# Optimization experiments

Hardware: AMD Instinct MI355X
Metric: run time of the kernel (lower is better)

## Reference

```python
import jax, jax.numpy as jnp
import numpy as np

N_NODES = 20000
N_EDGES = 320000
IN_CH = 256
HID_CH = 256   # 2 * out_channels
OUT_CH = 128


def gcn_conv(x, edge_index, W, b, n_nodes):
    """PyG GCNConv: linear transform, add self-loops, sym-normalized scatter-add."""
    x = x @ W  # [N, C_out]
    loop = jnp.arange(n_nodes, dtype=edge_index.dtype)
    row = jnp.concatenate([edge_index[0], loop])  # source nodes
    col = jnp.concatenate([edge_index[1], loop])  # destination nodes
    deg = jax.ops.segment_sum(jnp.ones_like(col, dtype=x.dtype), col,
                              num_segments=n_nodes)
    deg_inv_sqrt = jnp.where(deg > 0, jax.lax.rsqrt(deg), 0.0)
    norm = deg_inv_sqrt[row] * deg_inv_sqrt[col]  # [E+N]
    msg = x[row] * norm[:, None]                  # gather + scale
    out = jax.ops.segment_sum(msg, col, num_segments=n_nodes)  # scatter-add
    return out + b


def setup_inputs() -> dict:
    key = jax.random.key(0)
    k1, k2, k3, k4, k5 = jax.random.split(key, 5)
    doc_embeds = jax.random.normal(k1, (N_NODES, IN_CH), dtype=jnp.float32)
    edge_index = jax.random.randint(k2, (2, N_EDGES), 0, N_NODES, dtype=jnp.int64)
    # Glorot-style init for GCN weights, zero bias (PyG defaults)
    s1 = 1.0 / np.sqrt(IN_CH)
    s2 = 1.0 / np.sqrt(HID_CH)
    W1 = jax.random.uniform(k3, (IN_CH, HID_CH), jnp.float32, -s1, s1)
    b1 = jnp.zeros((HID_CH,), jnp.float32)
    W2 = jax.random.uniform(k4, (HID_CH, OUT_CH), jnp.float32, -s2, s2)
    b2 = jnp.zeros((OUT_CH,), jnp.float32)
    return {"doc_embeds": doc_embeds, "edge_index": edge_index,
            "W1": W1, "b1": b1, "W2": W2, "b2": b2}


def reference(doc_embeds, edge_index, W1, b1, W2, b2):
    n = doc_embeds.shape[0]
    x = jax.nn.relu(gcn_conv(doc_embeds, edge_index, W1, b1, n))
    x = gcn_conv(x, edge_index, W2, b2, n)
    return x
```

## Files before the change

### kernel.cpp

```cpp
#include <hip/hip_runtime.h>
#include <math.h>

#define N_NODES 20000
#define N_EDGES 320000
#define IN_CH   256
#define HID_CH  256
#define OUT_CH  128
#define CAP     64
#define GK      256

typedef __attribute__((ext_vector_type(8))) short short8;
typedef __attribute__((ext_vector_type(8))) unsigned short ushort8;
typedef __attribute__((ext_vector_type(4))) unsigned short ushort4v;
typedef __attribute__((ext_vector_type(2))) unsigned short ushort2v;
typedef __attribute__((ext_vector_type(4))) float floatx4;
typedef __attribute__((ext_vector_type(2))) float floatx2;
typedef __attribute__((ext_vector_type(2))) _Float16 half2v;

static __device__ __forceinline__ unsigned short f2bf(float f) {
    unsigned int u = __float_as_uint(f);
    u += 0x7FFFu + ((u >> 16) & 1u);
    return (unsigned short)(u >> 16);
}
static __device__ __forceinline__ float bf2f(unsigned short h) {
    return __uint_as_float(((unsigned int)h) << 16);
}

__global__ __launch_bounds__(256)
void prep_kernel(const float* __restrict__ W1, const float* __restrict__ W2,
                 unsigned short* __restrict__ W1thi, unsigned short* __restrict__ W1tlo,
                 unsigned short* __restrict__ W2thi, unsigned short* __restrict__ W2tlo,
                 const int* __restrict__ row, const int* __restrict__ col,
                 int* __restrict__ deg, unsigned short* __restrict__ srcs) {
    const int g = blockIdx.x * blockDim.x + threadIdx.x;
    const int gsz = gridDim.x * blockDim.x;
    for (int t = g; t < (IN_CH * HID_CH) / 16; t += gsz) {
        int n = t >> 4;
        int kc = (t & 15) * 16;
        ushort8 h0, l0, h1, l1;
#pragma unroll
        for (int j = 0; j < 8; ++j) {
            float x = W1[(size_t)(kc + j) * HID_CH + n];
            h0[j] = f2bf(x); l0[j] = f2bf(x - bf2f(h0[j]));
            float y = W1[(size_t)(kc + 8 + j) * HID_CH + n];
            h1[j] = f2bf(y); l1[j] = f2bf(y - bf2f(h1[j]));
        }
        *(ushort8*)(W1thi + (size_t)n * IN_CH + kc)     = h0;
        *(ushort8*)(W1thi + (size_t)n * IN_CH + kc + 8) = h1;
        *(ushort8*)(W1tlo + (size_t)n * IN_CH + kc)     = l0;
        *(ushort8*)(W1tlo + (size_t)n * IN_CH + kc + 8) = l1;
    }
    for (int t = g; t < (HID_CH * OUT_CH) / 16; t += gsz) {
        int n = t >> 4;
        int kc = (t & 15) * 16;
        ushort8 h0, l0, h1, l1;
#pragma unroll
        for (int j = 0; j < 8; ++j) {
            float x = W2[(size_t)(kc + j) * OUT_CH + n];
            h0[j] = f2bf(x); l0[j] = f2bf(x - bf2f(h0[j]));
            float y = W2[(size_t)(kc + 8 + j) * OUT_CH + n];
            h1[j] = f2bf(y); l1[j] = f2bf(y - bf2f(h1[j]));
        }
        *(ushort8*)(W2thi + (size_t)n * HID_CH + kc)     = h0;
        *(ushort8*)(W2thi + (size_t)n * HID_CH + kc + 8) = h1;
        *(ushort8*)(W2tlo + (size_t)n * HID_CH + kc)     = l0;
        *(ushort8*)(W2tlo + (size_t)n * HID_CH + kc + 8) = l1;
    }
    for (int i = g; i < N_EDGES; i += gsz) {
        int c = col[i];
        int r = row[i];
        int p = atomicAdd(&deg[c], 1);
        srcs[(size_t)c * CAP + p] = (unsigned short)r;
    }
}

template <int AMODE, int TN>
__global__ __launch_bounds__(256, 2)
void gemm_mfma_kernel(const float* __restrict__ Afp,
                      const unsigned short* __restrict__ Ahi, const unsigned short* __restrict__ Alo,
                      const unsigned short* __restrict__ Bthi, const unsigned short* __restrict__ Btlo,
                      const int* __restrict__ deg, _Float16* __restrict__ C, int M, int N) {
    constexpr int NJ = TN / 32;
    __shared__ unsigned short As[2][64][36];
    __shared__ unsigned short Bs[2][TN][36];
    const int tid = threadIdx.x;
    const int m0 = blockIdx.y * 64;
    const int lane = tid & 63;
    const int wave = tid >> 6;
    const int wr = (wave >> 1) * 32;
    const int wc = (wave & 1) * (TN / 2);
    const int lm = lane & 15;
    const int lk = (lane >> 4) * 8;

    floatx4 acc[2][NJ];
#pragma unroll
    for (int i = 0; i < 2; ++i)
#pragma unroll
        for (int j = 0; j < NJ; ++j) acc[i][j] = (floatx4){0.f, 0.f, 0.f, 0.f};

    const int ar  = tid >> 2;
    const int ako = (tid & 3) * 8;

    for (int k0 = 0; k0 < GK; k0 += 32) {
        {
            ushort8 vh = {}, vl = {};
            if (m0 + ar < M) {
                if (AMODE == 1) {
                    const float* ap = Afp + (size_t)(m0 + ar) * GK + k0 + ako;
                    float4 f0 = *(const float4*)ap;
                    float4 f1 = *(const float4*)(ap + 4);
                    float xs[8] = {f0.x, f0.y, f0.z, f0.w, f1.x, f1.y, f1.z, f1.w};
#pragma unroll
                    for (int j = 0; j < 8; ++j) {
                        vh[j] = f2bf(xs[j]);
                        vl[j] = f2bf(xs[j] - bf2f(vh[j]));
                    }
                } else {
                    size_t ga = (size_t)(m0 + ar) * GK + k0 + ako;
                    vh = *(const ushort8*)(Ahi + ga);
                    vl = *(const ushort8*)(Alo + ga);
                }
            }
            *(ushort8*)&As[0][ar][ako] = vh;
            *(ushort8*)&As[1][ar][ako] = vl;
        }
#pragma unroll
        for (int c = 0; c < TN / 64; ++c) {
            int ch = tid + c * 256;
            int r  = ch >> 2;
            int ko = (ch & 3) * 8;
            size_t gb = (size_t)r * GK + k0 + ko;
            *(ushort8*)&Bs[0][r][ko] = *(const ushort8*)(Bthi + gb);
            *(ushort8*)&Bs[1][r][ko] = *(const ushort8*)(Btlo + gb);
        }
        __syncthreads();

        short8 ah[2], al[2];
#pragma unroll
        for (int i = 0; i < 2; ++i) {
            ah[i] = *(const short8*)&As[0][wr + i * 16 + lm][lk];
            al[i] = *(const short8*)&As[1][wr + i * 16 + lm][lk];
        }
#pragma unroll
        for (int j = 0; j < NJ; ++j) {
            short8 bh = *(const short8*)&Bs[0][wc + j * 16 + lm][lk];
            short8 bl = *(const short8*)&Bs[1][wc + j * 16 + lm][lk];
#pragma unroll
            for (int i = 0; i < 2; ++i) {
                acc[i][j] = __builtin_amdgcn_mfma_f32_16x16x32_bf16(ah[i], bh, acc[i][j], 0, 0, 0);
                acc[i][j] = __builtin_amdgcn_mfma_f32_16x16x32_bf16(ah[i], bl, acc[i][j], 0, 0, 0);
                acc[i][j] = __builtin_amdgcn_mfma_f32_16x16x32_bf16(al[i], bh, acc[i][j], 0, 0, 0);
            }
        }
        __syncthreads();
    }

#pragma unroll
    for (int i = 0; i < 2; ++i) {
#pragma unroll
        for (int r = 0; r < 4; ++r) {
            int rowi = m0 + wr + i * 16 + (lane >> 4) * 4 + r;
            if (rowi < M) {
                float dr = 1.0f / sqrtf((float)(deg[rowi] + 1));
#pragma unroll
                for (int j = 0; j < NJ; ++j) {
                    C[(size_t)rowi * N + wc + j * 16 + lm] = (_Float16)(dr * acc[i][j][r]);
                }
            }
        }
    }
}

template <int C, int NSLICE, int MODE>
__global__ __launch_bounds__(256)
void gather_sliced_kernel(const _Float16* __restrict__ X, const int* __restrict__ deg,
                          const unsigned short* __restrict__ srcs,
                          const float* __restrict__ bias, float* __restrict__ outf,
                          unsigned short* __restrict__ outhi, unsigned short* __restrict__ outlo,
                          int n) {
    constexpr int SW = C / NSLICE;
    static_assert(SW == 64, "slice must be 64 channels");
    const int slice = blockIdx.x % NSLICE;
    const int ngrp  = blockIdx.x / NSLICE;
    const int wave = threadIdx.x >> 6;
    const int lane = threadIdx.x & 63;
    const int gg = lane >> 5;
    const int sl = lane & 31;
    const int node = ngrp * 8 + wave * 2 + gg;
    if (node >= n) return;
    const int choff = slice * SW + sl * 2;
    const size_t beg = (size_t)node * CAP;
    const int cnt = deg[node];

    float a0 = 0.f, a1 = 0.f;
    int e = 0;
    for (; e + 4 <= cnt; e += 4) {
        ushort4v s4 = *(const ushort4v*)(srcs + beg + e);
        half2v v0 = *(const half2v*)(X + (size_t)s4.x * C + choff);
        half2v v1 = *(const half2v*)(X + (size_t)s4.y * C + choff);
        half2v v2 = *(const half2v*)(X + (size_t)s4.z * C + choff);
        half2v v3 = *(const half2v*)(X + (size_t)s4.w * C + choff);
        a0 += (float)v0.x + (float)v1.x + (float)v2.x + (float)v3.x;
        a1 += (float)v0.y + (float)v1.y + (float)v2.y + (float)v3.y;
    }
    for (; e < cnt; ++e) {
        int r = srcs[beg + e];
        half2v v = *(const half2v*)(X + (size_t)r * C + choff);
        a0 += (float)v.x; a1 += (float)v.y;
    }

    const float dc = 1.0f / sqrtf((float)(cnt + 1));
    half2v vsh = *(const half2v*)(X + (size_t)node * C + choff);
    float2 bb = *(const float2*)(bias + choff);

    float o0 = dc * (a0 + (float)vsh.x) + bb.x;
    float o1 = dc * (a1 + (float)vsh.y) + bb.y;

    if constexpr (MODE == 1) {
        float r0 = fmaxf(o0, 0.f), r1 = fmaxf(o1, 0.f);
        ushort2v hv, lv;
        hv.x = f2bf(r0); lv.x = f2bf(r0 - bf2f(hv.x));
        hv.y = f2bf(r1); lv.y = f2bf(r1 - bf2f(hv.y));
        *(ushort2v*)(outhi + (size_t)node * C + choff) = hv;
        *(ushort2v*)(outlo + (size_t)node * C + choff) = lv;
    } else {
        floatx2 o = {o0, o1};
        __builtin_nontemporal_store(o, (floatx2*)(outf + (size_t)node * C + choff));
    }
}

extern "C" void kernel_launch(void* const* d_in, const int* in_sizes, int n_in,
                              void* d_out, int out_size, void* d_ws, size_t ws_size,
                              hipStream_t stream) {
    const float* doc_embeds = (const float*)d_in[0];
    const int*   edge_index = (const int*)d_in[1];
    const float* W1 = (const float*)d_in[2];
    const float* b1 = (const float*)d_in[3];
    const float* W2 = (const float*)d_in[4];
    const float* b2 = (const float*)d_in[5];
    float* out = (float*)d_out;

    const int* row = edge_index;
    const int* col = edge_index + N_EDGES;

    char* ws = (char*)d_ws;
    auto au = [](size_t x) { return (x + 255) / 256 * 256; };

    _Float16* X1s = (_Float16*)ws;      ws += au((size_t)N_NODES * HID_CH * 2);
    unsigned short* H1hi = (unsigned short*)ws; ws += au((size_t)N_NODES * HID_CH * 2);
    unsigned short* H1lo = (unsigned short*)ws; ws += au((size_t)N_NODES * HID_CH * 2);
    unsigned short* W1thi = (unsigned short*)ws; ws += au((size_t)IN_CH * HID_CH * 2);
    unsigned short* W1tlo = (unsigned short*)ws; ws += au((size_t)IN_CH * HID_CH * 2);
    unsigned short* W2thi = (unsigned short*)ws; ws += au((size_t)HID_CH * OUT_CH * 2);
    unsigned short* W2tlo = (unsigned short*)ws; ws += au((size_t)HID_CH * OUT_CH * 2);
    int*            deg   = (int*)ws;            ws += au((size_t)N_NODES * 4);
    unsigned short* srcs  = (unsigned short*)ws;

    hipMemsetAsync(deg, 0, (size_t)N_NODES * 4, stream);
    prep_kernel<<<(N_EDGES + 255) / 256, 256, 0, stream>>>(
        W1, W2, W1thi, W1tlo, W2thi, W2tlo, row, col, deg, srcs);

    {
        dim3 grid(1, (N_NODES + 63) / 64);
        gemm_mfma_kernel<1, 256><<<grid, 256, 0, stream>>>(
            doc_embeds, nullptr, nullptr, W1thi, W1tlo, deg, X1s, N_NODES, HID_CH);
    }
    gather_sliced_kernel<HID_CH, 4, 1><<<((N_NODES + 7) / 8) * 4, 256, 0, stream>>>(
        X1s, deg, srcs, b1, nullptr, H1hi, H1lo, N_NODES);

    {
        dim3 grid(1, (N_NODES + 63) / 64);
        gemm_mfma_kernel<3, 128><<<grid, 256, 0, stream>>>(
            nullptr, H1hi, H1lo, W2thi, W2tlo, deg, X1s, N_NODES, OUT_CH);
    }
    gather_sliced_kernel<OUT_CH, 2, 0><<<((N_NODES + 7) / 8) * 2, 256, 0, stream>>>(
        X1s, deg, srcs, b2, out, nullptr, nullptr, N_NODES);
}
```

Measured before the change: 176.3 us.

## Store layer-1 activations as single fp16 and narrow gather slices

The first aggregation now writes ReLU outputs as one fp16 tensor instead of a bf16 hi/lo pair, and the second GEMM loads fp16 and splits it into hi/lo bf16 in registers. This halves the intermediate write and read traffic. Separately, the gather kernels use 32-channel slices with 16 lanes per node and 4 nodes per wave, giving more nodes in flight per wave. The cost is fp16 rounding of the hidden activations, which loses precision and range compared with the previous split representation, plus shorter 4-byte loads per gathered row segment.

```diff
diff --git a/kernel.cpp b/kernel.cpp
--- a/kernel.cpp
+++ b/kernel.cpp
@@ -12,10 +12,10 @@
 typedef __attribute__((ext_vector_type(8))) short short8;
 typedef __attribute__((ext_vector_type(8))) unsigned short ushort8;
 typedef __attribute__((ext_vector_type(4))) unsigned short ushort4v;
-typedef __attribute__((ext_vector_type(2))) unsigned short ushort2v;
 typedef __attribute__((ext_vector_type(4))) float floatx4;
 typedef __attribute__((ext_vector_type(2))) float floatx2;
 typedef __attribute__((ext_vector_type(2))) _Float16 half2v;
+typedef __attribute__((ext_vector_type(8))) _Float16 half8;
 
 static __device__ __forceinline__ unsigned short f2bf(float f) {
     unsigned int u = __float_as_uint(f);
@@ -76,8 +76,7 @@
 
 template <int AMODE, int TN>
 __global__ __launch_bounds__(256, 2)
-void gemm_mfma_kernel(const float* __restrict__ Afp,
-                      const unsigned short* __restrict__ Ahi, const unsigned short* __restrict__ Alo,
+void gemm_mfma_kernel(const float* __restrict__ Afp, const _Float16* __restrict__ Ah,
                       const unsigned short* __restrict__ Bthi, const unsigned short* __restrict__ Btlo,
                       const int* __restrict__ deg, _Float16* __restrict__ C, int M, int N) {
     constexpr int NJ = TN / 32;
@@ -105,20 +104,22 @@
         {
             ushort8 vh = {}, vl = {};
             if (m0 + ar < M) {
+                float xs[8];
                 if (AMODE == 1) {
                     const float* ap = Afp + (size_t)(m0 + ar) * GK + k0 + ako;
                     float4 f0 = *(const float4*)ap;
                     float4 f1 = *(const float4*)(ap + 4);
-                    float xs[8] = {f0.x, f0.y, f0.z, f0.w, f1.x, f1.y, f1.z, f1.w};
-#pragma unroll
-                    for (int j = 0; j < 8; ++j) {
-                        vh[j] = f2bf(xs[j]);
-                        vl[j] = f2bf(xs[j] - bf2f(vh[j]));
-                    }
+                    xs[0] = f0.x; xs[1] = f0.y; xs[2] = f0.z; xs[3] = f0.w;
+                    xs[4] = f1.x; xs[5] = f1.y; xs[6] = f1.z; xs[7] = f1.w;
                 } else {
-                    size_t ga = (size_t)(m0 + ar) * GK + k0 + ako;
-                    vh = *(const ushort8*)(Ahi + ga);
-                    vl = *(const ushort8*)(Alo + ga);
+                    half8 hv = *(const half8*)(Ah + (size_t)(m0 + ar) * GK + k0 + ako);
+#pragma unroll
+                    for (int j = 0; j < 8; ++j) xs[j] = (float)hv[j];
+                }
+#pragma unroll
+                for (int j = 0; j < 8; ++j) {
+                    vh[j] = f2bf(xs[j]);
+                    vl[j] = f2bf(xs[j] - bf2f(vh[j]));
                 }
             }
             *(ushort8*)&As[0][ar][ako] = vh;
@@ -176,17 +177,16 @@
 void gather_sliced_kernel(const _Float16* __restrict__ X, const int* __restrict__ deg,
                           const unsigned short* __restrict__ srcs,
                           const float* __restrict__ bias, float* __restrict__ outf,
-                          unsigned short* __restrict__ outhi, unsigned short* __restrict__ outlo,
-                          int n) {
+                          _Float16* __restrict__ outh, int n) {
     constexpr int SW = C / NSLICE;
-    static_assert(SW == 64, "slice must be 64 channels");
+    static_assert(SW == 32, "slice must be 32 channels");
     const int slice = blockIdx.x % NSLICE;
     const int ngrp  = blockIdx.x / NSLICE;
     const int wave = threadIdx.x >> 6;
     const int lane = threadIdx.x & 63;
-    const int gg = lane >> 5;
-    const int sl = lane & 31;
-    const int node = ngrp * 8 + wave * 2 + gg;
+    const int g  = lane >> 4;
+    const int sl = lane & 15;
+    const int node = ngrp * 16 + wave * 4 + g;
     if (node >= n) return;
     const int choff = slice * SW + sl * 2;
     const size_t beg = (size_t)node * CAP;
@@ -217,12 +217,10 @@
     float o1 = dc * (a1 + (float)vsh.y) + bb.y;
 
     if constexpr (MODE == 1) {
-        float r0 = fmaxf(o0, 0.f), r1 = fmaxf(o1, 0.f);
-        ushort2v hv, lv;
-        hv.x = f2bf(r0); lv.x = f2bf(r0 - bf2f(hv.x));
-        hv.y = f2bf(r1); lv.y = f2bf(r1 - bf2f(hv.y));
-        *(ushort2v*)(outhi + (size_t)node * C + choff) = hv;
-        *(ushort2v*)(outlo + (size_t)node * C + choff) = lv;
+        half2v h;
+        h.x = (_Float16)fmaxf(o0, 0.f);
+        h.y = (_Float16)fmaxf(o1, 0.f);
+        *(half2v*)(outh + (size_t)node * C + choff) = h;
     } else {
         floatx2 o = {o0, o1};
         __builtin_nontemporal_store(o, (floatx2*)(outf + (size_t)node * C + choff));
@@ -244,17 +242,18 @@
     const int* col = edge_index + N_EDGES;
 
     char* ws = (char*)d_ws;
-    auto au = [](size_t x) { return (x + 255) / 256 * 256; };
-
-    _Float16* X1s = (_Float16*)ws;      ws += au((size_t)N_NODES * HID_CH * 2);
-    unsigned short* H1hi = (unsigned short*)ws; ws += au((size_t)N_NODES * HID_CH * 2);
-    unsigned short* H1lo = (unsigned short*)ws; ws += au((size_t)N_NODES * HID_CH * 2);
-    unsigned short* W1thi = (unsigned short*)ws; ws += au((size_t)IN_CH * HID_CH * 2);
-    unsigned short* W1tlo = (unsigned short*)ws; ws += au((size_t)IN_CH * HID_CH * 2);
-    unsigned short* W2thi = (unsigned short*)ws; ws += au((size_t)HID_CH * OUT_CH * 2);
-    unsigned short* W2tlo = (unsigned short*)ws; ws += au((size_t)HID_CH * OUT_CH * 2);
-    int*            deg   = (int*)ws;            ws += au((size_t)N_NODES * 4);
-    unsigned short* srcs  = (unsigned short*)ws;
+    auto align_up = [](size_t x) { return (x + 255) / 256 * 256; };
+
+    _Float16* X1s = (_Float16*)(ws);
+    _Float16* H1  = (_Float16*)(ws + align_up((size_t)N_NODES * HID_CH * 2));
+    _Float16* X2s = X1s;
+    char* meta = (char*)(ws + 2 * align_up((size_t)N_NODES * HID_CH * 2));
+    unsigned short* W1thi = (unsigned short*)(meta); meta += align_up((size_t)IN_CH * HID_CH * 2);
+    unsigned short* W1tlo = (unsigned short*)(meta); meta += align_up((size_t)IN_CH * HID_CH * 2);
+    unsigned short* W2thi = (unsigned short*)(meta); meta += align_up((size_t)HID_CH * OUT_CH * 2);
+    unsigned short* W2tlo = (unsigned short*)(meta); meta += align_up((size_t)HID_CH * OUT_CH * 2);
+    int*            deg   = (int*)(meta);            meta += align_up((size_t)N_NODES * 4);
+    unsigned short* srcs  = (unsigned short*)(meta);
 
     hipMemsetAsync(deg, 0, (size_t)N_NODES * 4, stream);
     prep_kernel<<<(N_EDGES + 255) / 256, 256, 0, stream>>>(
@@ -263,16 +262,16 @@
     {
         dim3 grid(1, (N_NODES + 63) / 64);
         gemm_mfma_kernel<1, 256><<<grid, 256, 0, stream>>>(
-            doc_embeds, nullptr, nullptr, W1thi, W1tlo, deg, X1s, N_NODES, HID_CH);
-    }
-    gather_sliced_kernel<HID_CH, 4, 1><<<((N_NODES + 7) / 8) * 4, 256, 0, stream>>>(
-        X1s, deg, srcs, b1, nullptr, H1hi, H1lo, N_NODES);
+            doc_embeds, nullptr, W1thi, W1tlo, deg, X1s, N_NODES, HID_CH);
+    }
+    gather_sliced_kernel<HID_CH, 8, 1><<<((N_NODES + 15) / 16) * 8, 256, 0, stream>>>(
+        X1s, deg, srcs, b1, nullptr, H1, N_NODES);
 
     {
         dim3 grid(1, (N_NODES + 63) / 64);
-        gemm_mfma_kernel<3, 128><<<grid, 256, 0, stream>>>(
-            nullptr, H1hi, H1lo, W2thi, W2tlo, deg, X1s, N_NODES, OUT_CH);
-    }
-    gather_sliced_kernel<OUT_CH, 2, 0><<<((N_NODES + 7) / 8) * 2, 256, 0, stream>>>(
-        X1s, deg, srcs, b2, out, nullptr, nullptr, N_NODES);
-}
+        gemm_mfma_kernel<2, 128><<<grid, 256, 0, stream>>>(
+            nullptr, H1, W2thi, W2tlo, deg, X2s, N_NODES, OUT_CH);
+    }
+    gather_sliced_kernel<OUT_CH, 4, 0><<<((N_NODES + 15) / 16) * 4, 256, 0, stream>>>(
+        X2s, deg, srcs, b2, out, nullptr, N_NODES);
+}
```

Measured after the change: 179.7 us. About the same (+1.9%).
